# Optimization experiments

Hardware: AMD Instinct MI355X
Metric: run time of the kernel (lower is better)

## Reference

```python
import jax, jax.numpy as jnp
import numpy as np

N_NODES = 50000
N_EDGES = 800000
D_IN = 64
D_RADIAL = 128


def setup_inputs() -> dict:
    key = jax.random.key(0)
    k1, k2, k3, k4, k5 = jax.random.split(key, 5)
    x = jax.random.normal(k1, (N_NODES, D_IN), dtype=jnp.float32)
    edge_basis = jax.random.normal(k2, (N_EDGES, D_RADIAL), dtype=jnp.float32)
    src = jax.random.randint(k3, (N_EDGES,), 0, N_NODES, dtype=jnp.int32)
    dst = jax.random.randint(k4, (N_EDGES,), 0, N_NODES, dtype=jnp.int32)
    # kaiming normal fan_in, linear nonlinearity: std = 1/sqrt(fan_in)
    W = jax.random.normal(k5, (D_IN, D_RADIAL), dtype=jnp.float32) / jnp.sqrt(
        jnp.float32(D_RADIAL))
    b = jnp.zeros((D_IN,), dtype=jnp.float32)
    return {"x": x, "edge_basis": edge_basis, "src": src, "dst": dst,
            "W": W, "b": b}


def reference(x, edge_basis, src, dst, W, b):
    # per-edge radial filter: Linear(d_radial -> d_in)  [E, d_in]
    filt = jnp.einsum('er,dr->ed', edge_basis, W) + b
    # gather source node features, multiply by filter  [E, d_in]
    m = x[src] * filt
    # scatter-sum messages into destination nodes      [N, d_in]
    h = jax.ops.segment_sum(m, dst, num_segments=x.shape[0])
    return h
```

## Files before the change

### kernel.cpp

```cpp
#include <hip/hip_runtime.h>

#define N_NODES  50000
#define N_EDGES  800000
#define D_IN     64
#define D_RADIAL 128
#define NTILES   (N_EDGES / 64)

typedef __bf16 bf16x8 __attribute__((ext_vector_type(8)));
typedef float  f32x4  __attribute__((ext_vector_type(4)));
typedef short  s16x8  __attribute__((ext_vector_type(8)));

__device__ inline unsigned int pack_bf16_pair(float lo, float hi) {
    return __builtin_amdgcn_perm(__float_as_uint(hi), __float_as_uint(lo), 0x07060302u);
}

__device__ inline short f2bf_rne(float f) {
    unsigned int u = __float_as_uint(f);
    u += 0x7FFFu + ((u >> 16) & 1u);
    return (short)(u >> 16);
}

__global__ __launch_bounds__(256) void edge_msg_kernel(
    const float* __restrict__ x,
    const float* __restrict__ eb,
    const int*   __restrict__ src,
    const int*   __restrict__ dst,
    const float* __restrict__ W,
    const float* __restrict__ bias_p,
    float*       __restrict__ out)
{
    const int lane = threadIdx.x & 63;
    const int wv   = threadIdx.x >> 6;
    const int l15  = lane & 15;
    const int quad = lane >> 4;

    bf16x8 wfrag[4][4];
    #pragma unroll
    for (int nt = 0; nt < 4; ++nt) {
        const int d = nt * 16 + l15;
        #pragma unroll
        for (int kt = 0; kt < 4; ++kt) {
            const float* p = W + d * D_RADIAL + kt * 32 + quad * 8;
            s16x8 s;
            #pragma unroll
            for (int j = 0; j < 8; ++j) s[j] = f2bf_rne(p[j]);
            wfrag[nt][kt] = __builtin_bit_cast(bf16x8, s);
        }
    }
    float bv[4];
    #pragma unroll
    for (int nt = 0; nt < 4; ++nt) bv[nt] = bias_p[nt * 16 + l15];

    for (int tile = blockIdx.x; tile < NTILES; tile += gridDim.x) {
        const int ebase = tile * 64 + wv * 16;

        f32x4 acc[4];
        #pragma unroll
        for (int nt = 0; nt < 4; ++nt) acc[nt] = (f32x4){0.f, 0.f, 0.f, 0.f};

        #pragma unroll
        for (int kt = 0; kt < 4; ++kt) {
            const float* p = eb + (long)(ebase + l15) * D_RADIAL + kt * 32 + quad * 8;
            f32x4 a0 = *(const f32x4*)(p);
            f32x4 a1 = *(const f32x4*)(p + 4);
            int4 packed;
            packed.x = pack_bf16_pair(a0[0], a0[1]);
            packed.y = pack_bf16_pair(a0[2], a0[3]);
            packed.z = pack_bf16_pair(a1[0], a1[1]);
            packed.w = pack_bf16_pair(a1[2], a1[3]);
            bf16x8 afrag = __builtin_bit_cast(bf16x8, packed);
            #pragma unroll
            for (int nt = 0; nt < 4; ++nt)
                acc[nt] = __builtin_amdgcn_mfma_f32_16x16x32_bf16(
                    afrag, wfrag[nt][kt], acc[nt], 0, 0, 0);
        }

        const int erow = ebase + quad * 4;
        #pragma unroll
        for (int reg = 0; reg < 4; ++reg) {
            const int e  = erow + reg;
            const int sv = src[e];
            const int dv = dst[e];
            const float* xrow = x   + (long)sv * D_IN;
            float*       orow = out + (long)dv * D_IN;
            #pragma unroll
            for (int nt = 0; nt < 4; ++nt) {
                const int d = nt * 16 + l15;
                const float val = (acc[nt][reg] + bv[nt]) * xrow[d];
                unsafeAtomicAdd(orow + d, val);
            }
        }
    }
}

extern "C" void kernel_launch(void* const* d_in, const int* in_sizes, int n_in,
                              void* d_out, int out_size, void* d_ws, size_t ws_size,
                              hipStream_t stream) {
    const float* x    = (const float*)d_in[0];
    const float* eb   = (const float*)d_in[1];
    const int*   src  = (const int*)d_in[2];
    const int*   dst  = (const int*)d_in[3];
    const float* W    = (const float*)d_in[4];
    const float* bias = (const float*)d_in[5];
    float* out = (float*)d_out;

    hipMemsetAsync(d_out, 0, (size_t)N_NODES * D_IN * sizeof(float), stream);

    edge_msg_kernel<<<1024, 256, 0, stream>>>(x, eb, src, dst, W, bias, out);
}
```

Measured before the change: 712.9 us.

## Replace float atomic scatter with CSR-sorted message buffer and segmented gather

Builds a destination-sorted layout on the device: a histogram of dst, a single-block prefix scan and an atomic rank assignment. The MFMA edge kernel then writes each message to its sorted slot, and a per-node gather kernel sums contiguous rows without float atomics. This aims to remove the 51M contended float atomic adds. The cost is about 200MB of extra workspace writes and reads plus several extra launches, including a serial single-block scan. If the workspace is too small, it falls back to the atomic kernel with a larger grid and a nontemporal load of dst.

```diff
diff --git a/kernel.cpp b/kernel.cpp
--- a/kernel.cpp
+++ b/kernel.cpp
@@ -6,6 +6,13 @@
 #define D_RADIAL 128
 #define NTILES   (N_EDGES / 64)
 
+#define M_OFF    0ull
+#define RANK_OFF 204800000ull
+#define CNT_OFF  208000000ull
+#define OFFS_OFF 208200000ull
+#define CUR_OFF  208400004ull
+#define WS_NEED  208600004ull
+
 typedef __bf16 bf16x8 __attribute__((ext_vector_type(8)));
 typedef float  f32x4  __attribute__((ext_vector_type(4)));
 typedef short  s16x8  __attribute__((ext_vector_type(8)));
@@ -13,21 +20,66 @@
 __device__ inline unsigned int pack_bf16_pair(float lo, float hi) {
     return __builtin_amdgcn_perm(__float_as_uint(hi), __float_as_uint(lo), 0x07060302u);
 }
-
 __device__ inline short f2bf_rne(float f) {
     unsigned int u = __float_as_uint(f);
     u += 0x7FFFu + ((u >> 16) & 1u);
     return (short)(u >> 16);
 }
 
-__global__ __launch_bounds__(256) void edge_msg_kernel(
+__global__ __launch_bounds__(256) void hist_kernel(const int* __restrict__ dst,
+                                                   int* __restrict__ counts) {
+    int i = blockIdx.x * 256 + threadIdx.x;
+    if (i < N_EDGES) atomicAdd(&counts[dst[i]], 1);
+}
+
+__global__ __launch_bounds__(1024) void scan_kernel(const int* __restrict__ counts,
+                                                    int* __restrict__ off,
+                                                    int* __restrict__ cursor) {
+    __shared__ int buf[1024];
+    __shared__ int base_s;
+    const int tid = threadIdx.x;
+    if (tid == 0) base_s = 0;
+    __syncthreads();
+    for (int start = 0; start < N_NODES; start += 1024) {
+        const int i = start + tid;
+        const int v = (i < N_NODES) ? counts[i] : 0;
+        buf[tid] = v;
+        __syncthreads();
+        #pragma unroll
+        for (int d = 1; d < 1024; d <<= 1) {
+            int t = (tid >= d) ? buf[tid - d] : 0;
+            __syncthreads();
+            buf[tid] += t;
+            __syncthreads();
+        }
+        const int incl = buf[tid];
+        const int base = base_s;
+        if (i < N_NODES) {
+            off[i]    = base + incl - v;
+            cursor[i] = base + incl - v;
+        }
+        __syncthreads();
+        if (tid == 1023) base_s = base + incl;
+        __syncthreads();
+    }
+    if (tid == 0) off[N_NODES] = base_s;
+}
+
+__global__ __launch_bounds__(256) void rank_kernel(const int* __restrict__ dst,
+                                                   int* __restrict__ cursor,
+                                                   int* __restrict__ rank) {
+    int i = blockIdx.x * 256 + threadIdx.x;
+    if (i < N_EDGES) rank[i] = atomicAdd(&cursor[dst[i]], 1);
+}
+
+__global__ __launch_bounds__(256) void edge_msg_csr_kernel(
     const float* __restrict__ x,
     const float* __restrict__ eb,
     const int*   __restrict__ src,
-    const int*   __restrict__ dst,
     const float* __restrict__ W,
     const float* __restrict__ bias_p,
-    float*       __restrict__ out)
+    const int*   __restrict__ rank,
+    float*       __restrict__ m)
 {
     const int lane = threadIdx.x & 63;
     const int wv   = threadIdx.x >> 6;
@@ -80,14 +132,102 @@
         for (int reg = 0; reg < 4; ++reg) {
             const int e  = erow + reg;
             const int sv = src[e];
-            const int dv = dst[e];
+            const int rk = rank[e];
+            const float* xrow = x + (long)sv * D_IN;
+            float*       mrow = m + (long)rk * D_IN;
+            #pragma unroll
+            for (int nt = 0; nt < 4; ++nt) {
+                const int d = nt * 16 + l15;
+                mrow[d] = (acc[nt][reg] + bv[nt]) * xrow[d];
+            }
+        }
+    }
+}
+
+__global__ __launch_bounds__(256) void gather_kernel(
+    const float* __restrict__ m,
+    const int*   __restrict__ off,
+    float*       __restrict__ out)
+{
+    const int lane = threadIdx.x & 63;
+    const int wv   = threadIdx.x >> 6;
+    const int n    = blockIdx.x * 4 + wv;
+    const int beg  = off[n];
+    const int end  = off[n + 1];
+
+    float a0 = 0.f, a1 = 0.f, a2 = 0.f, a3 = 0.f;
+    int j = beg;
+    for (; j + 4 <= end; j += 4) {
+        a0 += m[(long)(j + 0) * D_IN + lane];
+        a1 += m[(long)(j + 1) * D_IN + lane];
+        a2 += m[(long)(j + 2) * D_IN + lane];
+        a3 += m[(long)(j + 3) * D_IN + lane];
+    }
+    for (; j < end; ++j) a0 += m[(long)j * D_IN + lane];
+    out[(long)n * D_IN + lane] = (a0 + a1) + (a2 + a3);
+}
+
+__global__ __launch_bounds__(256) void edge_msg_atomic_kernel(
+    const float* __restrict__ x, const float* __restrict__ eb,
+    const int* __restrict__ src, const int* __restrict__ dst,
+    const float* __restrict__ W, const float* __restrict__ bias_p,
+    float* __restrict__ out)
+{
+    const int lane = threadIdx.x & 63;
+    const int wv   = threadIdx.x >> 6;
+    const int l15  = lane & 15;
+    const int quad = lane >> 4;
+
+    bf16x8 wfrag[4][4];
+    #pragma unroll
+    for (int nt = 0; nt < 4; ++nt) {
+        const int d = nt * 16 + l15;
+        #pragma unroll
+        for (int kt = 0; kt < 4; ++kt) {
+            const float* p = W + d * D_RADIAL + kt * 32 + quad * 8;
+            s16x8 s;
+            #pragma unroll
+            for (int j = 0; j < 8; ++j) s[j] = f2bf_rne(p[j]);
+            wfrag[nt][kt] = __builtin_bit_cast(bf16x8, s);
+        }
+    }
+    float bv[4];
+    #pragma unroll
+    for (int nt = 0; nt < 4; ++nt) bv[nt] = bias_p[nt * 16 + l15];
+
+    for (int tile = blockIdx.x; tile < NTILES; tile += gridDim.x) {
+        const int ebase = tile * 64 + wv * 16;
+        f32x4 acc[4];
+        #pragma unroll
+        for (int nt = 0; nt < 4; ++nt) acc[nt] = (f32x4){0.f, 0.f, 0.f, 0.f};
+        #pragma unroll
+        for (int kt = 0; kt < 4; ++kt) {
+            const float* p = eb + (long)(ebase + l15) * D_RADIAL + kt * 32 + quad * 8;
+            f32x4 a0 = *(const f32x4*)(p);
+            f32x4 a1 = *(const f32x4*)(p + 4);
+            int4 packed;
+            packed.x = pack_bf16_pair(a0[0], a0[1]);
+            packed.y = pack_bf16_pair(a0[2], a0[3]);
+            packed.z = pack_bf16_pair(a1[0], a1[1]);
+            packed.w = pack_bf16_pair(a1[2], a1[3]);
+            bf16x8 afrag = __builtin_bit_cast(bf16x8, packed);
+            #pragma unroll
+            for (int nt = 0; nt < 4; ++nt)
+                acc[nt] = __builtin_amdgcn_mfma_f32_16x16x32_bf16(
+                    afrag, wfrag[nt][kt], acc[nt], 0, 0, 0);
+        }
+        const int erow = ebase + quad * 4;
+        #pragma unroll
+        for (int reg = 0; reg < 4; ++reg) {
+            const int e  = erow + reg;
+            const int sv = src[e];
+            const int dv = __builtin_nontemporal_load(&dst[e]);
             const float* xrow = x   + (long)sv * D_IN;
             float*       orow = out + (long)dv * D_IN;
             #pragma unroll
             for (int nt = 0; nt < 4; ++nt) {
                 const int d = nt * 16 + l15;
-                const float val = (acc[nt][reg] + bv[nt]) * xrow[d];
-                unsafeAtomicAdd(orow + d, val);
+                unsafeAtomicAdd(orow + d, (acc[nt][reg] + bv[nt]) * xrow[d]);
             }
         }
     }
@@ -104,7 +244,23 @@
     const float* bias = (const float*)d_in[5];
     float* out = (float*)d_out;
 
-    hipMemsetAsync(d_out, 0, (size_t)N_NODES * D_IN * sizeof(float), stream);
-
-    edge_msg_kernel<<<1024, 256, 0, stream>>>(x, eb, src, dst, W, bias, out);
-}
+    if (ws_size < WS_NEED) {
+        hipMemsetAsync(d_out, 0, (size_t)N_NODES * D_IN * sizeof(float), stream);
+        edge_msg_atomic_kernel<<<2500, 256, 0, stream>>>(x, eb, src, dst, W, bias, out);
+        return;
+    }
+
+    char* ws = (char*)d_ws;
+    float* m      = (float*)(ws + M_OFF);
+    int*   rank   = (int*)  (ws + RANK_OFF);
+    int*   counts = (int*)  (ws + CNT_OFF);
+    int*   off    = (int*)  (ws + OFFS_OFF);
+    int*   cursor = (int*)  (ws + CUR_OFF);
+
+    hipMemsetAsync(counts, 0, (size_t)N_NODES * sizeof(int), stream);
+    hist_kernel<<<(N_EDGES + 255) / 256, 256, 0, stream>>>(dst, counts);
+    scan_kernel<<<1, 1024, 0, stream>>>(counts, off, cursor);
+    rank_kernel<<<(N_EDGES + 255) / 256, 256, 0, stream>>>(dst, cursor, rank);
+    edge_msg_csr_kernel<<<2500, 256, 0, stream>>>(x, eb, src, W, bias, rank, m);
+    gather_kernel<<<N_NODES / 4, 256, 0, stream>>>(m, off, out);
+}
```

After: 795.9 us. +11.6%, slower.
